# Kernel optimization log

Hardware: AMD Instinct MI355X
Metric: run time of the kernel (lower is better)

The kernel has to match this reference:

```python
import jax, jax.numpy as jnp
import numpy as np

D_MODEL = 256
D_STATE = 64
D_CONV = 4
EXPAND = 2
HEADDIM = 64
D_INNER = EXPAND * D_MODEL            # 512
NHEADS = D_INNER // HEADDIM           # 8
D_XBC = D_INNER + 2 * D_STATE         # 640 (x, B, C; ngroups=1)
D_IN_PROJ = 2 * D_INNER + 2 * D_STATE + NHEADS  # 1160


def setup_inputs() -> dict:
    key = jax.random.key(0)
    ks = jax.random.split(key, 8)
    x = jax.random.normal(ks[0], (64, 5000, 12), jnp.float32)
    W_in = jax.random.normal(ks[1], (D_MODEL, D_IN_PROJ), jnp.float32) * 0.02
    conv_w = jax.random.normal(ks[2], (D_XBC, D_CONV), jnp.float32) * 0.1
    conv_b = jnp.zeros((D_XBC,), jnp.float32)
    A_log = jnp.log(jax.random.uniform(ks[3], (NHEADS,), jnp.float32, 1.0, 16.0))
    dt_bias = jax.random.normal(ks[4], (NHEADS,), jnp.float32) * 0.1
    D = jnp.ones((NHEADS,), jnp.float32)
    norm_w = jnp.ones((D_INNER,), jnp.float32)
    W_out = jax.random.normal(ks[5], (D_INNER, D_MODEL), jnp.float32) * 0.02
    return {"x": x, "W_in": W_in, "conv_w": conv_w, "conv_b": conv_b,
            "A_log": A_log, "dt_bias": dt_bias, "D": D,
            "norm_w": norm_w, "W_out": W_out}


def _mamba2(u, W_in, conv_w, conv_b, A_log, dt_bias, D, norm_w, W_out):
    b, l, _ = u.shape
    zxbcdt = u @ W_in                                   # (b,l,1160)
    z = zxbcdt[..., :D_INNER]                           # (b,l,512)
    xBC = zxbcdt[..., D_INNER:D_INNER + D_XBC]          # (b,l,640)
    dt = zxbcdt[..., D_INNER + D_XBC:]                  # (b,l,8)
    # causal depthwise conv1d (kernel 4) + SiLU
    xp = jnp.pad(xBC, ((0, 0), (D_CONV - 1, 0), (0, 0)))
    xBC = sum(xp[:, k:k + l, :] * conv_w[:, k] for k in range(D_CONV)) + conv_b
    xBC = jax.nn.silu(xBC)
    xs = xBC[..., :D_INNER].reshape(b, l, NHEADS, HEADDIM)
    Bm = xBC[..., D_INNER:D_INNER + D_STATE]            # (b,l,64)
    Cm = xBC[..., D_INNER + D_STATE:]                   # (b,l,64)
    dt = jax.nn.softplus(dt + dt_bias)                  # (b,l,h)
    A = -jnp.exp(A_log)                                 # (h,)

    def step(h, inp):
        x_t, dt_t, B_t, C_t = inp                       # (b,h,p),(b,h),(b,n),(b,n)
        decay = jnp.exp(dt_t * A)                       # (b,h)
        h = h * decay[..., None, None] + (dt_t[..., None] * x_t)[..., None] * B_t[:, None, None, :]
        y = jnp.einsum('bhpn,bn->bhp', h, C_t)
        return h, y

    h0 = jnp.zeros((b, NHEADS, HEADDIM, D_STATE), u.dtype)
    _, ys = jax.lax.scan(step, h0, (xs.transpose(1, 0, 2, 3), dt.transpose(1, 0, 2),
                                    Bm.transpose(1, 0, 2), Cm.transpose(1, 0, 2)))
    y = ys.transpose(1, 0, 2, 3) + D[None, None, :, None] * xs   # D skip, per head
    y = y.reshape(b, l, D_INNER)
    # RMSNormGated: gate then rmsnorm
    y = y * jax.nn.silu(z)
    y = y * jax.lax.rsqrt(jnp.mean(y * y, axis=-1, keepdims=True) + 1e-5) * norm_w
    return y @ W_out                                    # (b,l,256)


def reference(x, W_in, conv_w, conv_b, A_log, dt_bias, D, norm_w, W_out):
    b = x.shape[0]
    u = x.reshape(b, 250, 240)                          # 'b (t p1) f -> b t (p1 f)'
    u = jnp.pad(u, ((0, 0), (0, 0), (0, D_MODEL - 240)))
    y = _mamba2(u, W_in, conv_w, conv_b, A_log, dt_bias, D, norm_w, W_out)
    y = jax.nn.selu(y)                                  # AlphaDropout is identity at eval
    y = y[..., :240]
    return y.reshape(b, 5000, 12)
```

## Files before the change

kernel.cpp:

```cpp
#include <hip/hip_runtime.h>
#include <cstdint>
#include <cstddef>

#define D_MODEL 256
#define D_STATE 64
#define HEADDIM 64
#define D_INNER 512
#define NHEADS 8
#define D_XBC 640
#define NPROJ 1160
#define ZXW 1152
#define BATCH 64
#define SEQ 250
#define ROWS (BATCH * SEQ)
#define KIN 240
#define KPAD 256
#define NPAD 1216
#define TPAD 256

typedef __bf16 bf16x8 __attribute__((ext_vector_type(8)));
typedef float f32x4 __attribute__((ext_vector_type(4)));

__device__ __forceinline__ float readlane_f(float v, int lane) {
    return __uint_as_float(__builtin_amdgcn_readlane(__float_as_uint(v), lane));
}
__device__ __forceinline__ float silu_f(float x) { return x * (1.f / (1.f + __expf(-x))); }
__device__ __forceinline__ unsigned short bf16_rne(float f) {
    unsigned int u = __float_as_uint(f);
    u += 0x7fff + ((u >> 16) & 1);
    return (unsigned short)(u >> 16);
}
__device__ __forceinline__ float bf2f(unsigned short u) {
    return __uint_as_float(((unsigned int)u) << 16);
}
__device__ __forceinline__ unsigned int pack2(float a, float b) {
    return (unsigned int)bf16_rne(a) | ((unsigned int)bf16_rne(b) << 16);
}

#define NA (ROWS * KPAD)
#define NB (NPAD * KPAD)
#define NW (D_MODEL * D_INNER)
__global__ __launch_bounds__(256) void cast_all_kernel(const float* __restrict__ x,
                                                       const float* __restrict__ Win,
                                                       const float* __restrict__ Wout,
                                                       unsigned short* __restrict__ a_bf,
                                                       unsigned short* __restrict__ bt_bf,
                                                       unsigned short* __restrict__ wt_bf) {
    int idx = blockIdx.x * 256 + threadIdx.x;
    if (idx < NA) {
        int row = idx >> 8, c = idx & 255;
        float v = (c < KIN) ? x[row * KIN + c] : 0.f;
        a_bf[idx] = bf16_rne(v);
    } else if (idx < NA + NB) {
        int r = idx - NA;
        int n = r >> 8, k = r & 255;
        float v = (n < NPROJ && k < KIN) ? Win[k * NPROJ + n] : 0.f;
        bt_bf[r] = bf16_rne(v);
    } else if (idx < NA + NB + NW) {
        int r = idx - NA - NB;
        int n = r & 255, k = r >> 8;
        wt_bf[n * D_INNER + k] = bf16_rne(Wout[k * D_MODEL + n]);
    }
}

#define SA 40
__global__ __launch_bounds__(256) void gemm1_mfma(const unsigned short* __restrict__ A,
                                                  const unsigned short* __restrict__ Bt,
                                                  unsigned short* __restrict__ Czx,
                                                  float* __restrict__ dtraw) {
    __shared__ unsigned short As[128 * SA];
    __shared__ unsigned short Bs[64 * SA];
    const int tid = threadIdx.x;
    const int lane = tid & 63, wave = tid >> 6;
    const int wm = wave >> 1, wn = wave & 1;
    const int q = lane >> 4, l15 = lane & 15;
    const int rowBase = blockIdx.y * 128, colBase = blockIdx.x * 64;
    f32x4 acc[4][2] = {};

    const int sr = tid >> 2;
    const int sc = (tid & 3) * 8;

    for (int k0 = 0; k0 < KPAD; k0 += 32) {
        *(uint4*)&As[sr * SA + sc] =
            *(const uint4*)&A[(size_t)(rowBase + sr) * KPAD + k0 + sc];
        *(uint4*)&As[(sr + 64) * SA + sc] =
            *(const uint4*)&A[(size_t)(rowBase + sr + 64) * KPAD + k0 + sc];
        *(uint4*)&Bs[sr * SA + sc] =
            *(const uint4*)&Bt[(size_t)(colBase + sr) * KPAD + k0 + sc];
        __syncthreads();

        bf16x8 bfr[2];
#pragma unroll
        for (int nt = 0; nt < 2; nt++)
            bfr[nt] = *(const bf16x8*)&Bs[(wn * 32 + nt * 16 + l15) * SA + q * 8];
#pragma unroll
        for (int mt = 0; mt < 4; mt++) {
            bf16x8 afr = *(const bf16x8*)&As[(wm * 64 + mt * 16 + l15) * SA + q * 8];
#pragma unroll
            for (int nt = 0; nt < 2; nt++)
                acc[mt][nt] = __builtin_amdgcn_mfma_f32_16x16x32_bf16(afr, bfr[nt],
                                                                      acc[mt][nt], 0, 0, 0);
        }
        __syncthreads();
    }
#pragma unroll
    for (int mt = 0; mt < 4; mt++) {
        int grow0 = rowBase + wm * 64 + mt * 16 + q * 4;
#pragma unroll
        for (int nt = 0; nt < 2; nt++) {
            int gcol = colBase + wn * 32 + nt * 16 + l15;
            if (gcol < ZXW) {
#pragma unroll
                for (int reg = 0; reg < 4; reg++) {
                    unsigned int u = bf16_rne(acc[mt][nt][reg]);
                    unsigned int partner = (unsigned int)__shfl_xor((int)u, 1, 64);
                    if ((l15 & 1) == 0)
                        *(unsigned int*)&Czx[(size_t)(grow0 + reg) * ZXW + gcol] =
                            u | (partner << 16);
                }
            } else if (gcol < NPROJ) {
#pragma unroll
                for (int reg = 0; reg < 4; reg++)
                    dtraw[(size_t)(grow0 + reg) * NHEADS + (gcol - ZXW)] = acc[mt][nt][reg];
            }
        }
    }
}

#define CT_IN_STR 68
#define CT_TR_STR 70
__global__ __launch_bounds__(256) void conv_kernel(const unsigned short* __restrict__ zxbc,
                                                   const float* __restrict__ dtraw,
                                                   const float* __restrict__ conv_w,
                                                   const float* __restrict__ conv_b,
                                                   const float* __restrict__ dt_bias,
                                                   unsigned short* __restrict__ xc_bf,
                                                   unsigned short* __restrict__ xcT_bf,
                                                   float* __restrict__ dtp) {
    const int b = blockIdx.x;
    const int t0 = blockIdx.z * 64;
    if (blockIdx.y == 10) {
        for (int it = threadIdx.x; it < 512; it += 256) {
            int h = it & 7;
            int t = t0 + (it >> 3);
            if (t < SEQ) {
                float v = dtraw[(size_t)(b * SEQ + t) * NHEADS + h] + dt_bias[h];
                dtp[(size_t)(b * SEQ + t) * NHEADS + h] =
                    (v > 20.f) ? v : __logf(1.f + __expf(v));
            }
        }
        return;
    }
    __shared__ float In[67 * CT_IN_STR];
    __shared__ unsigned short OutT[64 * CT_TR_STR];
    const int cg = blockIdx.y;
    const int tid = threadIdx.x;
    const int lane = tid & 63;
    const int w = tid >> 6;
    const int ch = cg * 64 + lane;

    for (int r = w; r < 67; r += 4) {
        int t = t0 - 3 + r;
        float v = (t >= 0 && t < SEQ)
                      ? bf2f(zxbc[(size_t)(b * SEQ + t) * ZXW + D_INNER + ch])
                      : 0.f;
        In[r * CT_IN_STR + lane] = v;
    }
    __syncthreads();
    const float w0 = conv_w[ch * 4 + 0], w1 = conv_w[ch * 4 + 1];
    const float w2 = conv_w[ch * 4 + 2], w3 = conv_w[ch * 4 + 3];
    const float bias = conv_b[ch];
    unsigned short vals[16];
#pragma unroll
    for (int i = 0; i < 16; i++) {
        int tt = w * 16 + i;
        float acc = fmaf(w3, In[(tt + 3) * CT_IN_STR + lane],
                    fmaf(w2, In[(tt + 2) * CT_IN_STR + lane],
                    fmaf(w1, In[(tt + 1) * CT_IN_STR + lane],
                    fmaf(w0, In[tt * CT_IN_STR + lane], bias))));
        float sv = silu_f(acc);
        unsigned short bv = (t0 + tt < SEQ) ? bf16_rne(sv) : (unsigned short)0;
        vals[i] = bv;
        OutT[lane * CT_TR_STR + tt] = bv;
    }
#pragma unroll
    for (int i = 0; i < 16; i++) {
        int tt = w * 16 + i;
        if (t0 + tt < SEQ)
            xc_bf[(size_t)(b * SEQ + t0 + tt) * D_XBC + ch] = vals[i];
    }
    __syncthreads();
    unsigned short* dstbase = xcT_bf + ((size_t)b * D_XBC + cg * 64) * TPAD + t0;
#pragma unroll
    for (int i = 0; i < 16; i++) {
        int c2 = w * 16 + i;
        dstbase[(size_t)c2 * TPAD + lane] = OutT[c2 * CT_TR_STR + lane];
    }
}

#define LSTR 72
__global__ __launch_bounds__(256) void scan_intra(const unsigned short* __restrict__ xc_bf,
                                                  const unsigned short* __restrict__ xcT_bf,
                                                  const float* __restrict__ dtp,
                                                  const float* __restrict__ A_log,
                                                  const float* __restrict__ Dvec,
                                                  unsigned short* __restrict__ yout_bf,
                                                  unsigned short* __restrict__ st_g) {
    __shared__ unsigned short C_l[64 * LSTR];
    __shared__ unsigned short BP_l[64 * LSTR];
    __shared__ unsigned short XT_l[64 * LSTR];
    __shared__ float cs_s[64], dts_s[64], fws_s[64];

    const int blk = blockIdx.x;
    const int bh = blk >> 2, c = blk & 3;
    const int b = bh >> 3, h = bh & 7;
    const int tid = threadIdx.x;
    const int lane = tid & 63, w = tid >> 6;
    const int q = lane >> 4, l15 = lane & 15;
    const int t0 = c * 64;
    const float A = -__expf(A_log[h]);
    const float Dh = Dvec[h];

    const int r = tid >> 2, c0 = (tid & 3) * 16;

    {
        if (t0 + r < SEQ) {
            const unsigned short* rowp = xc_bf + (size_t)(b * SEQ + t0 + r) * D_XBC;
            *(uint4*)&C_l[r * LSTR + c0] = *(const uint4*)&rowp[D_INNER + D_STATE + c0];
            *(uint4*)&C_l[r * LSTR + c0 + 8] =
                *(const uint4*)&rowp[D_INNER + D_STATE + c0 + 8];
            *(uint4*)&BP_l[r * LSTR + c0] = *(const uint4*)&rowp[D_INNER + c0];
            *(uint4*)&BP_l[r * LSTR + c0 + 8] = *(const uint4*)&rowp[D_INNER + c0 + 8];
        } else {
            uint4 z = {0, 0, 0, 0};
            *(uint4*)&C_l[r * LSTR + c0] = z;
            *(uint4*)&C_l[r * LSTR + c0 + 8] = z;
            *(uint4*)&BP_l[r * LSTR + c0] = z;
            *(uint4*)&BP_l[r * LSTR + c0 + 8] = z;
        }
        const unsigned short* xrow =
            xcT_bf + ((size_t)b * D_XBC + h * HEADDIM + r) * TPAD + t0;
        *(uint4*)&XT_l[r * LSTR + c0] = *(const uint4*)&xrow[c0];
        *(uint4*)&XT_l[r * LSTR + c0 + 8] = *(const uint4*)&xrow[c0 + 8];
    }
    uint4 braw0, braw1;
    {
        const unsigned short* brow =
            xcT_bf + ((size_t)b * D_XBC + D_INNER + r) * TPAD + t0 + c0;
        braw0 = *(const uint4*)&brow[0];
        braw1 = *(const uint4*)&brow[8];
    }
    if (w == 0) {
        int t = lane;
        float dtv = (t0 + t < SEQ) ? dtp[(size_t)(b * SEQ + t0 + t) * NHEADS + h] : 0.f;
        float csv = dtv * A;
#pragma unroll
        for (int o = 1; o < 64; o <<= 1) {
            float u = __shfl_up(csv, o, 64);
            if (lane >= o) csv += u;
        }
        float tot = readlane_f(csv, 63);
        cs_s[t] = csv;
        dts_s[t] = dtv;
        fws_s[t] = dtv * __expf(tot - csv);
    }
    __syncthreads();

    f32x4 g[4] = {};
#pragma unroll
    for (int k0 = 0; k0 < 64; k0 += 32) {
        bf16x8 ca = *(const bf16x8*)&C_l[(w * 16 + l15) * LSTR + k0 + q * 8];
#pragma unroll
        for (int nt = 0; nt < 4; nt++) {
            bf16x8 bb = *(const bf16x8*)&BP_l[(nt * 16 + l15) * LSTR + k0 + q * 8];
            g[nt] = __builtin_amdgcn_mfma_f32_16x16x32_bf16(ca, bb, g[nt], 0, 0, 0);
        }
    }
    __syncthreads();

    {
        unsigned short tmp[16];
        const unsigned short* rp = (const unsigned short*)&braw0;
#pragma unroll
        for (int j = 0; j < 8; j++) tmp[j] = bf16_rne(bf2f(rp[j]) * fws_s[c0 + j]);
        rp = (const unsigned short*)&braw1;
#pragma unroll
        for (int j = 0; j < 8; j++) tmp[8 + j] = bf16_rne(bf2f(rp[j]) * fws_s[c0 + 8 + j]);
        *(uint4*)&C_l[r * LSTR + c0] = *(uint4*)&tmp[0];
        *(uint4*)&C_l[r * LSTR + c0 + 8] = *(uint4*)&tmp[8];
    }
#pragma unroll
    for (int nt = 0; nt < 4; nt++) {
#pragma unroll
        for (int rr = 0; rr < 4; rr++) {
            int t = w * 16 + q * 4 + rr;
            int s = nt * 16 + l15;
            float pv = 0.f;
            if (s <= t) {
                pv = g[nt][rr] * __expf(cs_s[t] - cs_s[s]) * dts_s[s];
                if (s == t) pv += Dh;
            }
            unsigned int u = bf16_rne(pv);
            unsigned int partner = (unsigned int)__shfl_xor((int)u, 1, 64);
            if ((l15 & 1) == 0)
                *(unsigned int*)&BP_l[t * LSTR + nt * 16 + l15] = u | (partner << 16);
        }
    }
    __syncthreads();

    f32x4 y[4] = {};
#pragma unroll
    for (int k0 = 0; k0 < 64; k0 += 32) {
        bf16x8 pa = *(const bf16x8*)&BP_l[(w * 16 + l15) * LSTR + k0 + q * 8];
#pragma unroll
        for (int nt = 0; nt < 4; nt++) {
            bf16x8 xb = *(const bf16x8*)&XT_l[(nt * 16 + l15) * LSTR + k0 + q * 8];
            y[nt] = __builtin_amdgcn_mfma_f32_16x16x32_bf16(pa, xb, y[nt], 0, 0, 0);
        }
    }
    if (c < 3) {
        f32x4 st[4] = {};
#pragma unroll
        for (int k0 = 0; k0 < 64; k0 += 32) {
            bf16x8 xa = *(const bf16x8*)&XT_l[(w * 16 + l15) * LSTR + k0 + q * 8];
#pragma unroll
            for (int nt = 0; nt < 4; nt++) {
                bf16x8 bwb = *(const bf16x8*)&C_l[(nt * 16 + l15) * LSTR + k0 + q * 8];
                st[nt] = __builtin_amdgcn_mfma_f32_16x16x32_bf16(xa, bwb, st[nt], 0, 0, 0);
            }
        }
        unsigned short* stc = st_g + ((size_t)(bh * 3 + c)) * 4096;
#pragma unroll
        for (int nt = 0; nt < 4; nt++)
#pragma unroll
            for (int rr = 0; rr < 4; rr++) {
                unsigned int u = bf16_rne(st[nt][rr]);
                unsigned int partner = (unsigned int)__shfl_xor((int)u, 1, 64);
                if ((l15 & 1) == 0)
                    *(unsigned int*)&stc[(w * 16 + q * 4 + rr) * 64 + nt * 16 + l15] =
                        u | (partner << 16);
            }
    }
#pragma unroll
    for (int nt = 0; nt < 4; nt++)
#pragma unroll
        for (int rr = 0; rr < 4; rr++) {
            int t = w * 16 + q * 4 + rr;
            if (t0 + t < SEQ) {
                int p = nt * 16 + l15;
                unsigned int u = bf16_rne(y[nt][rr]);
                unsigned int partner = (unsigned int)__shfl_xor((int)u, 1, 64);
                if ((l15 & 1) == 0)
                    *(unsigned int*)&yout_bf[(size_t)(b * SEQ + t0 + t) * D_INNER +
                                             h * HEADDIM + p] = u | (partner << 16);
            }
        }
}

__global__ __launch_bounds__(256) void scan_inter(const unsigned short* __restrict__ xc_bf,
                                                  const float* __restrict__ dtp,
                                                  const float* __restrict__ A_log,
                                                  unsigned short* __restrict__ yout_bf,
                                                  const unsigned short* __restrict__ st_g) {
    __shared__ unsigned short C_l[64 * LSTR];
    __shared__ unsigned short h_l[64 * LSTR];
    __shared__ float cs_s[64];
    __shared__ float csum[4];

    const int blk = blockIdx.x;
    const int bh = blk / 3, c = (blk - bh * 3) + 1;
    const int b = bh >> 3, h = bh & 7;
    const int tid = threadIdx.x;
    const int lane = tid & 63, w = tid >> 6;
    const int q = lane >> 4, l15 = lane & 15;
    const int t0 = c * 64;
    const float A = -__expf(A_log[h]);

    {
        int t = lane;
        int gt = w * 64 + t;
        float dtv = (gt < SEQ) ? dtp[(size_t)(b * SEQ + gt) * NHEADS + h] : 0.f;
        float csv = dtv * A;
#pragma unroll
        for (int o = 1; o < 64; o <<= 1) {
            float u = __shfl_up(csv, o, 64);
            if (lane >= o) csv += u;
        }
        if (w == c) cs_s[t] = csv;
        if (lane == 63) csum[w] = csv;
    }
    {
        int r = tid >> 2, c0 = (tid & 3) * 16;
        if (t0 + r < SEQ) {
            const unsigned short* rowp = xc_bf + (size_t)(b * SEQ + t0 + r) * D_XBC;
            *(uint4*)&C_l[r * LSTR + c0] = *(const uint4*)&rowp[D_INNER + D_STATE + c0];
            *(uint4*)&C_l[r * LSTR + c0 + 8] =
                *(const uint4*)&rowp[D_INNER + D_STATE + c0 + 8];
        } else {
            uint4 z = {0, 0, 0, 0};
            *(uint4*)&C_l[r * LSTR + c0] = z;
            *(uint4*)&C_l[r * LSTR + c0 + 8] = z;
        }
    }
    __syncthreads();

    {
        float wgt[3];
        for (int cp = 0; cp < c; cp++) {
            float s = 0.f;
            for (int j = cp + 1; j < c; j++) s += csum[j];
            wgt[cp] = __expf(s);
        }
        const unsigned short* stb = st_g + (size_t)bh * 3 * 4096;
        for (int i = tid; i < 4096; i += 256) {
            float acc = 0.f;
            for (int cp = 0; cp < c; cp++) acc += wgt[cp] * bf2f(stb[cp * 4096 + i]);
            h_l[(i >> 6) * LSTR + (i & 63)] = bf16_rne(acc);
        }
    }
    __syncthreads();

    f32x4 in[4] = {};
#pragma unroll
    for (int k0 = 0; k0 < 64; k0 += 32) {
        bf16x8 ca = *(const bf16x8*)&C_l[(w * 16 + l15) * LSTR + k0 + q * 8];
#pragma unroll
        for (int nt = 0; nt < 4; nt++) {
            bf16x8 hb = *(const bf16x8*)&h_l[(nt * 16 + l15) * LSTR + k0 + q * 8];
            in[nt] = __builtin_amdgcn_mfma_f32_16x16x32_bf16(ca, hb, in[nt], 0, 0, 0);
        }
    }
#pragma unroll
    for (int nt = 0; nt < 4; nt++)
#pragma unroll
        for (int r = 0; r < 4; r++) {
            int t = w * 16 + q * 4 + r;
            if (t0 + t < SEQ) {
                int p = nt * 16 + l15;
                size_t ai = (size_t)(b * SEQ + t0 + t) * D_INNER + h * HEADDIM + p;
                float alpha = __expf(cs_s[t]);
                float nv = bf2f(yout_bf[ai]) + alpha * in[nt][r];
                unsigned int u = bf16_rne(nv);
                unsigned int partner = (unsigned int)__shfl_xor((int)u, 1, 64);
                if ((l15 & 1) == 0)
                    *(unsigned int*)&yout_bf[ai] = u | (partner << 16);
            }
        }
}

__global__ __launch_bounds__(256) void gemm2_fused(const unsigned short* __restrict__ yout_bf,
                                                   const unsigned short* __restrict__ zxbc,
                                                   const unsigned short* __restrict__ Bt,
                                                   const float* __restrict__ norm_w,
                                                   float* __restrict__ out) {
    __shared__ unsigned short As[32 * SA];
    __shared__ unsigned short Bs[256 * SA];
    __shared__ float rms_s[32];
    const int tid = threadIdx.x;
    const int lane = tid & 63;
    const int wn = tid >> 6;
    const int q = lane >> 4, l15 = lane & 15;
    const int rowBase = blockIdx.x * 32;
    f32x4 acc[2][4] = {};

    const int tr = tid >> 3;
    const int tk = (tid & 7) * 4;

    const unsigned short* yrow = yout_bf + (size_t)(rowBase + tr) * D_INNER + tk;
    const unsigned short* zrow = zxbc + (size_t)(rowBase + tr) * ZXW + tk;
    float ssq = 0.f;

    for (int k0 = 0; k0 < D_INNER; k0 += 32) {
        uint2 yp = *(const uint2*)&yrow[k0];
        uint2 zp = *(const uint2*)&zrow[k0];
        float4 nw = *(const float4*)&norm_w[k0 + tk];
        const unsigned short* ys = (const unsigned short*)&yp;
        const unsigned short* zs = (const unsigned short*)&zp;
        float g0 = bf2f(ys[0]) * silu_f(bf2f(zs[0]));
        float g1 = bf2f(ys[1]) * silu_f(bf2f(zs[1]));
        float g2 = bf2f(ys[2]) * silu_f(bf2f(zs[2]));
        float g3 = bf2f(ys[3]) * silu_f(bf2f(zs[3]));
        ssq = fmaf(g0, g0, ssq);
        ssq = fmaf(g1, g1, ssq);
        ssq = fmaf(g2, g2, ssq);
        ssq = fmaf(g3, g3, ssq);
        uint2 pk;
        pk.x = pack2(g0 * nw.x, g1 * nw.y);
        pk.y = pack2(g2 * nw.z, g3 * nw.w);
        *(uint2*)&As[tr * SA + tk] = pk;
        const unsigned short* brow = Bt + (size_t)tid * D_INNER + k0;
        *(uint4*)&Bs[tid * SA + 0] = *(const uint4*)&brow[0];
        *(uint4*)&Bs[tid * SA + 8] = *(const uint4*)&brow[8];
        *(uint4*)&Bs[tid * SA + 16] = *(const uint4*)&brow[16];
        *(uint4*)&Bs[tid * SA + 24] = *(const uint4*)&brow[24];
        __syncthreads();

        bf16x8 bfr[4];
#pragma unroll
        for (int nt = 0; nt < 4; nt++)
            bfr[nt] = *(const bf16x8*)&Bs[(wn * 64 + nt * 16 + l15) * SA + q * 8];
#pragma unroll
        for (int mt = 0; mt < 2; mt++) {
            bf16x8 afr = *(const bf16x8*)&As[(mt * 16 + l15) * SA + q * 8];
#pragma unroll
            for (int nt = 0; nt < 4; nt++)
                acc[mt][nt] = __builtin_amdgcn_mfma_f32_16x16x32_bf16(afr, bfr[nt],
                                                                      acc[mt][nt], 0, 0, 0);
        }
        __syncthreads();
    }
    ssq += __shfl_xor(ssq, 1, 64);
    ssq += __shfl_xor(ssq, 2, 64);
    ssq += __shfl_xor(ssq, 4, 64);
    if ((tid & 7) == 0) rms_s[tr] = rsqrtf(ssq * (1.f / 512.f) + 1e-5f);
    __syncthreads();

    const float SC = 1.0507009873554805f, AL = 1.6732632423543772f;
#pragma unroll
    for (int mt = 0; mt < 2; mt++) {
        int lrow0 = mt * 16 + q * 4;
#pragma unroll
        for (int nt = 0; nt < 4; nt++) {
            int gcol = wn * 64 + nt * 16 + l15;
            if (gcol < 240) {
#pragma unroll
                for (int reg = 0; reg < 4; reg++) {
                    float v = acc[mt][nt][reg] * rms_s[lrow0 + reg];
                    v = (v > 0.f) ? SC * v : SC * AL * (__expf(v) - 1.f);
                    out[(size_t)(rowBase + lrow0 + reg) * 240 + gcol] = v;
                }
            }
        }
    }
}

extern "C" void kernel_launch(void* const* d_in, const int* in_sizes, int n_in,
                              void* d_out, int out_size, void* d_ws, size_t ws_size,
                              hipStream_t stream) {
    const float* x = (const float*)d_in[0];
    const float* W_in = (const float*)d_in[1];
    const float* conv_w = (const float*)d_in[2];
    const float* conv_b = (const float*)d_in[3];
    const float* A_log = (const float*)d_in[4];
    const float* dt_bias = (const float*)d_in[5];
    const float* Dv = (const float*)d_in[6];
    const float* norm_w = (const float*)d_in[7];
    const float* W_out = (const float*)d_in[8];
    float* out = (float*)d_out;

    unsigned short* us = (unsigned short*)d_ws;
    unsigned short* zxbc_bf = us;
    unsigned short* xc_bf = zxbc_bf + (size_t)ROWS * ZXW;
    unsigned short* xcT_bf = xc_bf + (size_t)ROWS * D_XBC;
    unsigned short* yout_bf = xcT_bf + (size_t)BATCH * D_XBC * TPAD;
    unsigned short* st_g = yout_bf + (size_t)ROWS * D_INNER;
    unsigned short* bt_bf = st_g + (size_t)512 * 3 * 4096;
    unsigned short* wt_bf = bt_bf + (size_t)NPAD * KPAD;
    float* dtraw = (float*)(wt_bf + (size_t)D_MODEL * D_INNER);
    float* dtp = dtraw + (size_t)ROWS * NHEADS;
    unsigned short* a_bf = (unsigned short*)(dtp + (size_t)ROWS * NHEADS);

    int cast_total = NA + NB + NW;
    cast_all_kernel<<<dim3((cast_total + 255) / 256), 256, 0, stream>>>(x, W_in, W_out,
                                                                        a_bf, bt_bf, wt_bf);

    gemm1_mfma<<<dim3(NPAD / 64, ROWS / 128), 256, 0, stream>>>(a_bf, bt_bf, zxbc_bf, dtraw);

    conv_kernel<<<dim3(BATCH, 11, 4), 256, 0, stream>>>(zxbc_bf, dtraw, conv_w, conv_b,
                                                        dt_bias, xc_bf, xcT_bf, dtp);

    scan_intra<<<dim3(BATCH * NHEADS * 4), 256, 0, stream>>>(xc_bf, xcT_bf, dtp, A_log, Dv,
                                                             yout_bf, st_g);

    scan_inter<<<dim3(BATCH * NHEADS * 3), 256, 0, stream>>>(xc_bf, dtp, A_log,
                                                             yout_bf, st_g);

    gemm2_fused<<<dim3(ROWS / 32), 256, 0, stream>>>(yout_bf, zxbc_bf, wt_bf, norm_w, out);
}
```

Baseline: 209.9 us.

## Widen gemm1 tile to 128x128 and load tiles with global_load_lds

The input-projection GEMM now uses 128x128 output tiles instead of 128x64, so each wave computes 4x4 MFMA tiles and the A tile is reused across twice as many columns. Tile staging switches from register round-trips to direct global-to-LDS loads (global_load_lds, 16 bytes per lane), which requires an unpadded 32-wide LDS layout. NPAD is raised to 1280 so the column count divides the new tile width, which adds some padded columns of wasted MFMA work. The unpadded LDS rows may cause bank conflicts on fragment reads, and the larger tile halves the number of blocks in the grid.

```diff
diff --git a/kernel.cpp b/kernel.cpp
--- a/kernel.cpp
+++ b/kernel.cpp
@@ -15,11 +15,14 @@
 #define ROWS (BATCH * SEQ)
 #define KIN 240
 #define KPAD 256
-#define NPAD 1216
+#define NPAD 1280
 #define TPAD 256
 
 typedef __bf16 bf16x8 __attribute__((ext_vector_type(8)));
 typedef float f32x4 __attribute__((ext_vector_type(4)));
+
+typedef __attribute__((address_space(1))) const void gv_t;
+typedef __attribute__((address_space(3))) void lv_t;
 
 __device__ __forceinline__ float readlane_f(float v, int lane) {
     return __uint_as_float(__builtin_amdgcn_readlane(__float_as_uint(v), lane));
@@ -63,41 +66,45 @@
     }
 }
 
-#define SA 40
 __global__ __launch_bounds__(256) void gemm1_mfma(const unsigned short* __restrict__ A,
                                                   const unsigned short* __restrict__ Bt,
                                                   unsigned short* __restrict__ Czx,
                                                   float* __restrict__ dtraw) {
-    __shared__ unsigned short As[128 * SA];
-    __shared__ unsigned short Bs[64 * SA];
+    __shared__ unsigned short As[128 * 32];
+    __shared__ unsigned short Bs[128 * 32];
     const int tid = threadIdx.x;
     const int lane = tid & 63, wave = tid >> 6;
     const int wm = wave >> 1, wn = wave & 1;
     const int q = lane >> 4, l15 = lane & 15;
-    const int rowBase = blockIdx.y * 128, colBase = blockIdx.x * 64;
-    f32x4 acc[4][2] = {};
+    const int rowBase = blockIdx.y * 128, colBase = blockIdx.x * 128;
+    f32x4 acc[4][4] = {};
 
     const int sr = tid >> 2;
     const int sc = (tid & 3) * 8;
 
+    const unsigned short* gA = A + (size_t)(rowBase + sr) * KPAD + sc;
+    const unsigned short* gB = Bt + (size_t)(colBase + sr) * KPAD + sc;
+    unsigned short* lA = &As[sr * 32 + sc];
+    unsigned short* lB = &Bs[sr * 32 + sc];
+
     for (int k0 = 0; k0 < KPAD; k0 += 32) {
-        *(uint4*)&As[sr * SA + sc] =
-            *(const uint4*)&A[(size_t)(rowBase + sr) * KPAD + k0 + sc];
-        *(uint4*)&As[(sr + 64) * SA + sc] =
-            *(const uint4*)&A[(size_t)(rowBase + sr + 64) * KPAD + k0 + sc];
-        *(uint4*)&Bs[sr * SA + sc] =
-            *(const uint4*)&Bt[(size_t)(colBase + sr) * KPAD + k0 + sc];
+        __builtin_amdgcn_global_load_lds((gv_t*)(gA + k0), (lv_t*)lA, 16, 0, 0);
+        __builtin_amdgcn_global_load_lds((gv_t*)(gA + 64 * KPAD + k0),
+                                         (lv_t*)(lA + 64 * 32), 16, 0, 0);
+        __builtin_amdgcn_global_load_lds((gv_t*)(gB + k0), (lv_t*)lB, 16, 0, 0);
+        __builtin_amdgcn_global_load_lds((gv_t*)(gB + 64 * KPAD + k0),
+                                         (lv_t*)(lB + 64 * 32), 16, 0, 0);
         __syncthreads();
 
-        bf16x8 bfr[2];
-#pragma unroll
-        for (int nt = 0; nt < 2; nt++)
-            bfr[nt] = *(const bf16x8*)&Bs[(wn * 32 + nt * 16 + l15) * SA + q * 8];
+        bf16x8 bfr[4];
+#pragma unroll
+        for (int nt = 0; nt < 4; nt++)
+            bfr[nt] = *(const bf16x8*)&Bs[(wn * 64 + nt * 16 + l15) * 32 + q * 8];
 #pragma unroll
         for (int mt = 0; mt < 4; mt++) {
-            bf16x8 afr = *(const bf16x8*)&As[(wm * 64 + mt * 16 + l15) * SA + q * 8];
-#pragma unroll
-            for (int nt = 0; nt < 2; nt++)
+            bf16x8 afr = *(const bf16x8*)&As[(wm * 64 + mt * 16 + l15) * 32 + q * 8];
+#pragma unroll
+            for (int nt = 0; nt < 4; nt++)
                 acc[mt][nt] = __builtin_amdgcn_mfma_f32_16x16x32_bf16(afr, bfr[nt],
                                                                       acc[mt][nt], 0, 0, 0);
         }
@@ -107,8 +114,8 @@
     for (int mt = 0; mt < 4; mt++) {
         int grow0 = rowBase + wm * 64 + mt * 16 + q * 4;
 #pragma unroll
-        for (int nt = 0; nt < 2; nt++) {
-            int gcol = colBase + wn * 32 + nt * 16 + l15;
+        for (int nt = 0; nt < 4; nt++) {
+            int gcol = colBase + wn * 64 + nt * 16 + l15;
             if (gcol < ZXW) {
 #pragma unroll
                 for (int reg = 0; reg < 4; reg++) {
@@ -448,13 +455,14 @@
         }
 }
 
+#define SA 40
 __global__ __launch_bounds__(256) void gemm2_fused(const unsigned short* __restrict__ yout_bf,
                                                    const unsigned short* __restrict__ zxbc,
                                                    const unsigned short* __restrict__ Bt,
                                                    const float* __restrict__ norm_w,
                                                    float* __restrict__ out) {
-    __shared__ unsigned short As[32 * SA];
-    __shared__ unsigned short Bs[256 * SA];
+    __shared__ unsigned short As2[32 * SA];
+    __shared__ unsigned short Bs2[256 * SA];
     __shared__ float rms_s[32];
     const int tid = threadIdx.x;
     const int lane = tid & 63;
@@ -487,21 +495,21 @@
         uint2 pk;
         pk.x = pack2(g0 * nw.x, g1 * nw.y);
         pk.y = pack2(g2 * nw.z, g3 * nw.w);
-        *(uint2*)&As[tr * SA + tk] = pk;
+        *(uint2*)&As2[tr * SA + tk] = pk;
         const unsigned short* brow = Bt + (size_t)tid * D_INNER + k0;
-        *(uint4*)&Bs[tid * SA + 0] = *(const uint4*)&brow[0];
-        *(uint4*)&Bs[tid * SA + 8] = *(const uint4*)&brow[8];
-        *(uint4*)&Bs[tid * SA + 16] = *(const uint4*)&brow[16];
-        *(uint4*)&Bs[tid * SA + 24] = *(const uint4*)&brow[24];
+        *(uint4*)&Bs2[tid * SA + 0] = *(const uint4*)&brow[0];
+        *(uint4*)&Bs2[tid * SA + 8] = *(const uint4*)&brow[8];
+        *(uint4*)&Bs2[tid * SA + 16] = *(const uint4*)&brow[16];
+        *(uint4*)&Bs2[tid * SA + 24] = *(const uint4*)&brow[24];
         __syncthreads();
 
         bf16x8 bfr[4];
 #pragma unroll
         for (int nt = 0; nt < 4; nt++)
-            bfr[nt] = *(const bf16x8*)&Bs[(wn * 64 + nt * 16 + l15) * SA + q * 8];
+            bfr[nt] = *(const bf16x8*)&Bs2[(wn * 64 + nt * 16 + l15) * SA + q * 8];
 #pragma unroll
         for (int mt = 0; mt < 2; mt++) {
-            bf16x8 afr = *(const bf16x8*)&As[(mt * 16 + l15) * SA + q * 8];
+            bf16x8 afr = *(const bf16x8*)&As2[(mt * 16 + l15) * SA + q * 8];
 #pragma unroll
             for (int nt = 0; nt < 4; nt++)
                 acc[mt][nt] = __builtin_amdgcn_mfma_f32_16x16x32_bf16(afr, bfr[nt],
@@ -564,7 +572,7 @@
     cast_all_kernel<<<dim3((cast_total + 255) / 256), 256, 0, stream>>>(x, W_in, W_out,
                                                                         a_bf, bt_bf, wt_bf);
 
-    gemm1_mfma<<<dim3(NPAD / 64, ROWS / 128), 256, 0, stream>>>(a_bf, bt_bf, zxbc_bf, dtraw);
+    gemm1_mfma<<<dim3(NPAD / 128, ROWS / 128), 256, 0, stream>>>(a_bf, bt_bf, zxbc_bf, dtraw);
 
     conv_kernel<<<dim3(BATCH, 11, 4), 256, 0, stream>>>(zxbc_bf, dtraw, conv_w, conv_b,
                                                         dt_bias, xc_bf, xcT_bf, dtp);
```

Measured after the change: 205.7 us. -2.0%, faster.
